# Kernel optimization log

Hardware: AMD Instinct MI355X
Metric: run time of the kernel (lower is better)

Reference implementation:

```python
import jax, jax.numpy as jnp
import numpy as np

DS_STEPS = 9
MAX_RND = 1.0
SMOKE_AUG = 0.5
SIZE = 512


def diamond_square(key, steps=DS_STEPS, max_rnd=MAX_RND):
    """Vectorized, faithful port of f_seed_grid + f_dsmain.

    Notes on faithfulness to the original code:
      - interior 'temp' reads in the diamond step resolve to the cell's own
        center (i_min + half == i_mid), exactly as in the original (buggy)
        indexing, so the interior averages double-count the center.
      - the '== 0' guards mean top/left edge midpoints are only written for
        the first row/column of cells (fresh zeros); elsewhere they were
        already written as bottom/right edges of neighboring cells.
    All per-level updates read only square-step (center) and coarser-level
    values, so each level is fully parallel.
    """
    N = 2 ** steps + 1
    hm = jnp.zeros((N, N), jnp.float32)
    corners = jax.random.uniform(jax.random.fold_in(key, 1000), (4,), minval=-1.0, maxval=1.0)
    hm = (hm.at[0, 0].set(corners[0]).at[0, -1].set(corners[1])
            .at[-1, 0].set(corners[2]).at[-1, -1].set(corners[3]))
    L = N - 1  # shape_length
    for level in range(steps):
        g = 2 ** level          # grid_split
        h = L // 2              # half_v_grid_size
        r = max_rnd / (level + 1)
        ks = jax.random.split(jax.random.fold_in(key, level), 5)
        lows = jnp.arange(g) * L
        highs = lows + L
        mids = lows + h
        # corner reads (set at coarser levels / seeds)
        nw = hm[lows[:, None], lows[None, :]]
        ne = hm[lows[:, None], highs[None, :]]
        sw = hm[highs[:, None], lows[None, :]]
        se = hm[highs[:, None], highs[None, :]]
        # square step: cell centers
        centers = (nw + ne + sw + se) / 4.0 + jax.random.uniform(ks[0], (g, g), minval=-r, maxval=r)
        hm = hm.at[mids[:, None], mids[None, :]].set(centers)
        # diamond step (all reads from post-square values)
        # top row (only i_min==0 cells pass the ==0 guard); temp = hm[max_index-h, j_mid] = centers[g-1, j]
        top = (centers[0, :] + hm[0, lows] + hm[0, highs] + centers[g - 1, :]) / 4.0 \
              + jax.random.uniform(ks[1], (g,), minval=-r, maxval=r)
        # left col (only j_min==0 cells); temp = hm[i_mid, max_index-h] = centers[i, g-1]
        left = (centers[:, 0] + hm[lows, 0] + hm[highs, 0] + centers[:, g - 1]) / 4.0 \
               + jax.random.uniform(ks[2], (g,), minval=-r, maxval=r)
        # right edges of every cell; interior temp == own center, boundary temp = centers[i, 0]
        temp_r = jnp.where(jnp.arange(g)[None, :] < g - 1, centers, centers[:, :1])
        right = (centers + ne + se + temp_r) / 4.0 + jax.random.uniform(ks[3], (g, g), minval=-r, maxval=r)
        # bottom edges of every cell; interior temp == own center, boundary temp = centers[0, j]
        temp_b = jnp.where(jnp.arange(g)[:, None] < g - 1, centers, centers[:1, :])
        bottom = (centers + sw + se + temp_b) / 4.0 + jax.random.uniform(ks[4], (g, g), minval=-r, maxval=r)
        hm = hm.at[0, mids].set(top)
        hm = hm.at[mids, 0].set(left)
        hm = hm.at[mids[:, None], highs[None, :]].set(right)
        hm = hm.at[highs[:, None], mids[None, :]].set(bottom)
        L //= 2
    return hm


def make_smoke_noise(key):
    hm = diamond_square(key)
    noise = (hm - hm.min()) / (hm.max() - hm.min())          # [513, 513] in [0,1]
    noise = jax.image.resize(noise, (SIZE, SIZE), method="bilinear")
    return noise * SMOKE_AUG                                  # [H, W]


def setup_inputs() -> dict:
    key = jax.random.key(0)
    img = jax.random.uniform(key, (32, 3, 512, 512), dtype=jnp.float32)
    return {"img": img}


def reference(img) -> jnp.ndarray:
    rn = make_smoke_noise(jax.random.key(42))                 # [H, W]
    rn = rn[None, None]                                       # broadcast over [B, C, H, W]
    return jnp.clip(img * (1.0 - rn) + rn, 0.0, 1.0)
```

## Files before the change

kernel.cpp:

```cpp
#include <hip/hip_runtime.h>

struct KP { unsigned a, b; };

__host__ __device__ constexpr unsigned rotl32(unsigned x, int d) {
  return (x << d) | (x >> (32 - d));
}

__host__ __device__ constexpr KP tf2x32(unsigned k0, unsigned k1, unsigned x0, unsigned x1) {
  unsigned k2 = k0 ^ k1 ^ 0x1BD11BDAu;
  unsigned v0 = x0 + k0;
  unsigned v1 = x1 + k1;
  const int R[5][4] = {{13,15,26,6},{17,29,16,24},{13,15,26,6},{17,29,16,24},{13,15,26,6}};
  const unsigned KI[5][2] = {{k1, k2 + 1u},{k2, k0 + 2u},{k0, k1 + 3u},{k1, k2 + 4u},{k2, k0 + 5u}};
  for (int g = 0; g < 5; ++g) {
    for (int r = 0; r < 4; ++r) {
      v0 += v1;
      v1 = rotl32(v1, R[g][r]);
      v1 ^= v0;
    }
    v0 += KI[g][0];
    v1 += KI[g][1];
  }
  return KP{v0, v1};
}

struct AllKeys {
  unsigned lk[9][5][2];
  unsigned ck[2];
};

__host__ __device__ constexpr AllKeys make_keys() {
  AllKeys K{};
  for (int l = 0; l < 9; ++l) {
    KP base = tf2x32(0u, 42u, 0u, (unsigned)l);
    for (int m = 0; m < 5; ++m) {
      KP s = tf2x32(base.a, base.b, 0u, (unsigned)m);
      K.lk[l][m][0] = s.a;
      K.lk[l][m][1] = s.b;
    }
  }
  KP ck = tf2x32(0u, 42u, 0u, 1000u);
  K.ck[0] = ck.a;
  K.ck[1] = ck.b;
  return K;
}

constexpr AllKeys KEYS = make_keys();

#define NG 513

__device__ inline unsigned rbits(unsigned k0, unsigned k1, unsigned i) {
  KP o = tf2x32(k0, k1, 0u, i);
  return o.a ^ o.b;
}

__device__ inline float bits_to_u(unsigned b, float r) {
  float u = __uint_as_float((b >> 9) | 0x3f800000u) - 1.0f;
  return fmaxf(-r, u * (2.0f * r) - r);
}

__device__ inline float draw_u(const unsigned* kk, unsigned i, float r) {
  return bits_to_u(rbits(kk[0], kk[1], i), r);
}

__device__ inline float cell_center(const float* hm, int level, int g, int L,
                                    int a, int b, float r) {
  int lo_i = a * L, hi_i = lo_i + L, lo_j = b * L, hi_j = lo_j + L;
  float nw = hm[lo_i * NG + lo_j], ne = hm[lo_i * NG + hi_j];
  float sw = hm[hi_i * NG + lo_j], se = hm[hi_i * NG + hi_j];
  return (nw + ne + sw + se) * 0.25f +
         draw_u(KEYS.lk[level][0], (unsigned)(a * g + b), r);
}

__device__ inline void do_cell(float* hm, int level, int i, int j) {
  int g = 1 << level;
  int L = 512 >> level;
  int h = L >> 1;
  float r = 1.0f / (float)(level + 1);
  int lo_i = i * L, hi_i = lo_i + L, mi_i = lo_i + h;
  int lo_j = j * L, hi_j = lo_j + L, mi_j = lo_j + h;
  float nw = hm[lo_i * NG + lo_j], ne = hm[lo_i * NG + hi_j];
  float sw = hm[hi_i * NG + lo_j], se = hm[hi_i * NG + hi_j];
  unsigned m = (unsigned)(i * g + j);

  float c = (nw + ne + sw + se) * 0.25f + draw_u(KEYS.lk[level][0], m, r);
  hm[mi_i * NG + mi_j] = c;

  float tr = (j < g - 1) ? c : cell_center(hm, level, g, L, i, 0, r);
  float right = (c + ne + se + tr) * 0.25f + draw_u(KEYS.lk[level][3], m, r);
  hm[mi_i * NG + hi_j] = right;

  float tb = (i < g - 1) ? c : cell_center(hm, level, g, L, 0, j, r);
  float bottom = (c + sw + se + tb) * 0.25f + draw_u(KEYS.lk[level][4], m, r);
  hm[hi_i * NG + mi_j] = bottom;

  if (i == 0) {
    float cg1 = (g == 1) ? c : cell_center(hm, level, g, L, g - 1, j, r);
    float top = (c + hm[lo_j] + hm[hi_j] + cg1) * 0.25f +
                draw_u(KEYS.lk[level][1], (unsigned)j, r);
    hm[mi_j] = top;
  }
  if (j == 0) {
    float cg1 = (g == 1) ? c : cell_center(hm, level, g, L, i, g - 1, r);
    float left = (c + hm[lo_i * NG] + hm[hi_i * NG] + cg1) * 0.25f +
                 draw_u(KEYS.lk[level][2], (unsigned)i, r);
    hm[mi_i * NG] = left;
  }
}

__global__ void k_ds_small(float* hm, unsigned* mmx) {
  int tid = threadIdx.x;
  if (tid == 0) {
#pragma unroll
    for (int q = 0; q < 4; ++q) {
      float v = bits_to_u(rbits(KEYS.ck[0], KEYS.ck[1], (unsigned)q), 1.0f);
      int y = (q >> 1) ? 512 : 0;
      int x = (q & 1) ? 512 : 0;
      hm[y * NG + x] = v;
    }
    mmx[0] = 0xFFFFFFFFu;
    mmx[1] = 0u;
  }
  __syncthreads();
  for (int lvl = 0; lvl <= 5; ++lvl) {
    int g = 1 << lvl;
    if (tid < g * g) do_cell(hm, lvl, tid >> lvl, tid & (g - 1));
    __syncthreads();
  }
}

__global__ void k_level(float* hm, int level) {
  int g = 1 << level;
  int gt = blockIdx.x * blockDim.x + threadIdx.x;
  do_cell(hm, level, gt >> level, gt & (g - 1));
}

__device__ inline unsigned enc_f(float f) {
  unsigned u = __float_as_uint(f);
  return (u & 0x80000000u) ? ~u : (u | 0x80000000u);
}
__device__ inline float dec_f(unsigned e) {
  unsigned u = (e & 0x80000000u) ? (e & 0x7FFFFFFFu) : ~e;
  return __uint_as_float(u);
}

__global__ void k_minmax(const float* hm, unsigned* mmx) {
  int gtid = blockIdx.x * blockDim.x + threadIdx.x;
  int nthreads = gridDim.x * blockDim.x;
  float mn = 3.4e38f, mx = -3.4e38f;
  for (int idx = gtid; idx < NG * NG; idx += nthreads) {
    float v = hm[idx];
    mn = fminf(mn, v);
    mx = fmaxf(mx, v);
  }
#pragma unroll
  for (int off = 32; off >= 1; off >>= 1) {
    mn = fminf(mn, __shfl_down(mn, off, 64));
    mx = fmaxf(mx, __shfl_down(mx, off, 64));
  }
  if ((threadIdx.x & 63) == 0) {
    atomicMin(&mmx[0], enc_f(mn));
    atomicMax(&mmx[1], enc_f(mx));
  }
}

__global__ void k_noise(const float* hm, const unsigned* mmx, float* rn) {
  int o = blockIdx.x * blockDim.x + threadIdx.x;
  int oy = o >> 9, ox = o & 511;
  const float csc = 512.0f / 513.0f;
  float dx = (float)(2 * ox + 1) * (1.0f / 1024.0f);
  float wx0 = 1.0f - dx * csc;
  float wx1 = 1.0f - (1.0f - dx) * csc;
  float sx = wx0 + wx1;
  wx0 /= sx; wx1 /= sx;
  float dy = (float)(2 * oy + 1) * (1.0f / 1024.0f);
  float wy0 = 1.0f - dy * csc;
  float wy1 = 1.0f - (1.0f - dy) * csc;
  float sy = wy0 + wy1;
  wy0 /= sy; wy1 /= sy;
  const float* r0 = hm + oy * NG + ox;
  float v = wy0 * (wx0 * r0[0] + wx1 * r0[1]) + wy1 * (wx0 * r0[NG] + wx1 * r0[NG + 1]);
  float mn = dec_f(mmx[0]), mx = dec_f(mmx[1]);
  rn[o] = 0.5f * ((v - mn) / (mx - mn));
}

__global__ void k_apply(const float4* __restrict__ img, const float* __restrict__ rn,
                        float4* __restrict__ out) {
  int t = blockIdx.x * blockDim.x + threadIdx.x;
  int pos4 = t & ((512 * 512 / 4) - 1);
  float4 a = img[t];
  float4 n = reinterpret_cast<const float4*>(rn)[pos4];
  float4 o;
  o.x = fminf(fmaxf(a.x * (1.0f - n.x) + n.x, 0.0f), 1.0f);
  o.y = fminf(fmaxf(a.y * (1.0f - n.y) + n.y, 0.0f), 1.0f);
  o.z = fminf(fmaxf(a.z * (1.0f - n.z) + n.z, 0.0f), 1.0f);
  o.w = fminf(fmaxf(a.w * (1.0f - n.w) + n.w, 0.0f), 1.0f);
  out[t] = o;
}

__global__ void k_apply_direct(const float* __restrict__ img, const float* __restrict__ hm,
                               const unsigned* __restrict__ mmx, float* __restrict__ out) {
  int t = blockIdx.x * blockDim.x + threadIdx.x;
  int pos = t & (512 * 512 - 1);
  int oy = pos >> 9, ox = pos & 511;
  const float csc = 512.0f / 513.0f;
  float dx = (float)(2 * ox + 1) * (1.0f / 1024.0f);
  float wx0 = 1.0f - dx * csc;
  float wx1 = 1.0f - (1.0f - dx) * csc;
  float sx = wx0 + wx1;
  wx0 /= sx; wx1 /= sx;
  float dy = (float)(2 * oy + 1) * (1.0f / 1024.0f);
  float wy0 = 1.0f - dy * csc;
  float wy1 = 1.0f - (1.0f - dy) * csc;
  float sy = wy0 + wy1;
  wy0 /= sy; wy1 /= sy;
  const float* r0 = hm + oy * NG + ox;
  float v = wy0 * (wx0 * r0[0] + wx1 * r0[1]) + wy1 * (wx0 * r0[NG] + wx1 * r0[NG + 1]);
  float mn = dec_f(mmx[0]), mx = dec_f(mmx[1]);
  float rnv = 0.5f * ((v - mn) / (mx - mn));
  float a = img[t];
  out[t] = fminf(fmaxf(a * (1.0f - rnv) + rnv, 0.0f), 1.0f);
}

extern "C" void kernel_launch(void* const* d_in, const int* in_sizes, int n_in,
                              void* d_out, int out_size, void* d_ws, size_t ws_size,
                              hipStream_t stream) {
  const float* img = (const float*)d_in[0];
  float* out = (float*)d_out;
  unsigned char* ws = (unsigned char*)d_ws;

  const size_t RN_BYTES = 512 * 512 * sizeof(float);
  const size_t HM_BYTES = NG * NG * sizeof(float);
  const size_t need_full = 16 + RN_BYTES + HM_BYTES;

  unsigned* mmx = (unsigned*)ws;
  bool use_rn = (ws_size >= need_full);
  float* rn = (float*)(ws + 16);
  float* hm = use_rn ? (float*)(ws + 16 + RN_BYTES) : (float*)(ws + 16);

  hipLaunchKernelGGL(k_ds_small, dim3(1), dim3(1024), 0, stream, hm, mmx);
  hipLaunchKernelGGL(k_level, dim3(16), dim3(256), 0, stream, hm, 6);
  hipLaunchKernelGGL(k_level, dim3(64), dim3(256), 0, stream, hm, 7);
  hipLaunchKernelGGL(k_level, dim3(256), dim3(256), 0, stream, hm, 8);
  hipLaunchKernelGGL(k_minmax, dim3(64), dim3(256), 0, stream, hm, mmx);

  const int total = 32 * 3 * 512 * 512;
  if (use_rn) {
    hipLaunchKernelGGL(k_noise, dim3(512 * 512 / 256), dim3(256), 0, stream, hm, mmx, rn);
    hipLaunchKernelGGL(k_apply, dim3(total / 4 / 256), dim3(256), 0, stream,
                       (const float4*)img, rn, (float4*)out);
  } else {
    hipLaunchKernelGGL(k_apply_direct, dim3(total / 256), dim3(256), 0, stream,
                       img, hm, mmx, out);
  }
}
```

Before: 218.0 us.

## Fuse min/max into diamond-square levels and noise resize into apply kernel

Each diamond-square cell now tracks the running min and max of the values it writes. A wave shuffle, shared-memory and atomic reduction at the end of each level kernel replaces the separate full-grid min/max pass. Level 6 is folded into the single-block small-level kernel, and the bilinear resize plus normalization is computed inline in a float4 apply kernel, which removes the intermediate noise buffer and two launches. The cost is that the bilinear weights and unaligned heightmap loads are recomputed for every batch and channel in the bandwidth-bound apply pass, and level 6 now runs on a single workgroup.

Measured after the change: 227.5 us. 4.4% more time.

```diff
diff --git a/kernel.cpp b/kernel.cpp
--- a/kernel.cpp
+++ b/kernel.cpp
@@ -63,6 +63,15 @@
   return bits_to_u(rbits(kk[0], kk[1], i), r);
 }
 
+__device__ inline unsigned enc_f(float f) {
+  unsigned u = __float_as_uint(f);
+  return (u & 0x80000000u) ? ~u : (u | 0x80000000u);
+}
+__device__ inline float dec_f(unsigned e) {
+  unsigned u = (e & 0x80000000u) ? (e & 0x7FFFFFFFu) : ~e;
+  return __uint_as_float(u);
+}
+
 __device__ inline float cell_center(const float* hm, int level, int g, int L,
                                     int a, int b, float r) {
   int lo_i = a * L, hi_i = lo_i + L, lo_j = b * L, hi_j = lo_j + L;
@@ -72,7 +81,8 @@
          draw_u(KEYS.lk[level][0], (unsigned)(a * g + b), r);
 }
 
-__device__ inline void do_cell(float* hm, int level, int i, int j) {
+__device__ inline void do_cell(float* hm, int level, int i, int j,
+                               float& mn, float& mx) {
   int g = 1 << level;
   int L = 512 >> level;
   int h = L >> 1;
@@ -85,141 +95,127 @@
 
   float c = (nw + ne + sw + se) * 0.25f + draw_u(KEYS.lk[level][0], m, r);
   hm[mi_i * NG + mi_j] = c;
+  mn = fminf(mn, c); mx = fmaxf(mx, c);
 
   float tr = (j < g - 1) ? c : cell_center(hm, level, g, L, i, 0, r);
   float right = (c + ne + se + tr) * 0.25f + draw_u(KEYS.lk[level][3], m, r);
   hm[mi_i * NG + hi_j] = right;
+  mn = fminf(mn, right); mx = fmaxf(mx, right);
 
   float tb = (i < g - 1) ? c : cell_center(hm, level, g, L, 0, j, r);
   float bottom = (c + sw + se + tb) * 0.25f + draw_u(KEYS.lk[level][4], m, r);
   hm[hi_i * NG + mi_j] = bottom;
+  mn = fminf(mn, bottom); mx = fmaxf(mx, bottom);
 
   if (i == 0) {
     float cg1 = (g == 1) ? c : cell_center(hm, level, g, L, g - 1, j, r);
     float top = (c + hm[lo_j] + hm[hi_j] + cg1) * 0.25f +
                 draw_u(KEYS.lk[level][1], (unsigned)j, r);
     hm[mi_j] = top;
+    mn = fminf(mn, top); mx = fmaxf(mx, top);
   }
   if (j == 0) {
     float cg1 = (g == 1) ? c : cell_center(hm, level, g, L, i, g - 1, r);
     float left = (c + hm[lo_i * NG] + hm[hi_i * NG] + cg1) * 0.25f +
                  draw_u(KEYS.lk[level][2], (unsigned)i, r);
     hm[mi_i * NG] = left;
-  }
-}
-
-__global__ void k_ds_small(float* hm, unsigned* mmx) {
-  int tid = threadIdx.x;
-  if (tid == 0) {
-#pragma unroll
-    for (int q = 0; q < 4; ++q) {
-      float v = bits_to_u(rbits(KEYS.ck[0], KEYS.ck[1], (unsigned)q), 1.0f);
-      int y = (q >> 1) ? 512 : 0;
-      int x = (q & 1) ? 512 : 0;
-      hm[y * NG + x] = v;
-    }
-    mmx[0] = 0xFFFFFFFFu;
-    mmx[1] = 0u;
-  }
-  __syncthreads();
-  for (int lvl = 0; lvl <= 5; ++lvl) {
-    int g = 1 << lvl;
-    if (tid < g * g) do_cell(hm, lvl, tid >> lvl, tid & (g - 1));
-    __syncthreads();
-  }
-}
-
-__global__ void k_level(float* hm, int level) {
-  int g = 1 << level;
-  int gt = blockIdx.x * blockDim.x + threadIdx.x;
-  do_cell(hm, level, gt >> level, gt & (g - 1));
-}
-
-__device__ inline unsigned enc_f(float f) {
-  unsigned u = __float_as_uint(f);
-  return (u & 0x80000000u) ? ~u : (u | 0x80000000u);
-}
-__device__ inline float dec_f(unsigned e) {
-  unsigned u = (e & 0x80000000u) ? (e & 0x7FFFFFFFu) : ~e;
-  return __uint_as_float(u);
-}
-
-__global__ void k_minmax(const float* hm, unsigned* mmx) {
-  int gtid = blockIdx.x * blockDim.x + threadIdx.x;
-  int nthreads = gridDim.x * blockDim.x;
-  float mn = 3.4e38f, mx = -3.4e38f;
-  for (int idx = gtid; idx < NG * NG; idx += nthreads) {
-    float v = hm[idx];
-    mn = fminf(mn, v);
-    mx = fmaxf(mx, v);
-  }
+    mn = fminf(mn, left); mx = fmaxf(mx, left);
+  }
+}
+
+template <int NWAVES>
+__device__ inline void block_minmax_atomic(float mn, float mx, unsigned* mmx) {
+  __shared__ float smn[NWAVES], smx[NWAVES];
 #pragma unroll
   for (int off = 32; off >= 1; off >>= 1) {
     mn = fminf(mn, __shfl_down(mn, off, 64));
     mx = fmaxf(mx, __shfl_down(mx, off, 64));
   }
-  if ((threadIdx.x & 63) == 0) {
+  int lane = threadIdx.x & 63, w = threadIdx.x >> 6;
+  if (lane == 0) { smn[w] = mn; smx[w] = mx; }
+  __syncthreads();
+  if (threadIdx.x == 0) {
+#pragma unroll
+    for (int q = 1; q < NWAVES; ++q) {
+      mn = fminf(mn, smn[q]);
+      mx = fmaxf(mx, smx[q]);
+    }
     atomicMin(&mmx[0], enc_f(mn));
     atomicMax(&mmx[1], enc_f(mx));
   }
 }
 
-__global__ void k_noise(const float* hm, const unsigned* mmx, float* rn) {
-  int o = blockIdx.x * blockDim.x + threadIdx.x;
-  int oy = o >> 9, ox = o & 511;
+__global__ void k_ds_small(float* hm, unsigned* mmx) {
+  int tid = threadIdx.x;
+  float mn = 3.4e38f, mx = -3.4e38f;
+  if (tid == 0) {
+    mmx[0] = 0xFFFFFFFFu;
+    mmx[1] = 0u;
+  }
+  if (tid < 4) {
+    float v = bits_to_u(rbits(KEYS.ck[0], KEYS.ck[1], (unsigned)tid), 1.0f);
+    int y = (tid >> 1) ? 512 : 0;
+    int x = (tid & 1) ? 512 : 0;
+    hm[y * NG + x] = v;
+    mn = fminf(mn, v); mx = fmaxf(mx, v);
+  }
+  __syncthreads();
+  for (int lvl = 0; lvl <= 5; ++lvl) {
+    int g = 1 << lvl;
+    if (tid < g * g) do_cell(hm, lvl, tid >> lvl, tid & (g - 1), mn, mx);
+    __syncthreads();
+  }
+  for (int c = tid; c < 64 * 64; c += 1024)
+    do_cell(hm, 6, c >> 6, c & 63, mn, mx);
+  block_minmax_atomic<16>(mn, mx, mmx);
+}
+
+__global__ void k_level(float* hm, unsigned* mmx, int level) {
+  int g = 1 << level;
+  int gt = blockIdx.x * blockDim.x + threadIdx.x;
+  float mn = 3.4e38f, mx = -3.4e38f;
+  do_cell(hm, level, gt >> level, gt & (g - 1), mn, mx);
+  block_minmax_atomic<4>(mn, mx, mmx);
+}
+
+__global__ void k_apply(const float4* __restrict__ img, const float* __restrict__ hm,
+                        const unsigned* __restrict__ mmx, float4* __restrict__ out) {
+  int t = blockIdx.x * blockDim.x + threadIdx.x;
+  int pos4 = t & (512 * 512 / 4 - 1);
+  int oy = pos4 >> 7;
+  int ox = (pos4 & 127) << 2;
+
+  float mn = dec_f(mmx[0]);
+  float scale = 0.5f / (dec_f(mmx[1]) - mn);
+
   const float csc = 512.0f / 513.0f;
-  float dx = (float)(2 * ox + 1) * (1.0f / 1024.0f);
-  float wx0 = 1.0f - dx * csc;
-  float wx1 = 1.0f - (1.0f - dx) * csc;
-  float sx = wx0 + wx1;
-  wx0 /= sx; wx1 /= sx;
   float dy = (float)(2 * oy + 1) * (1.0f / 1024.0f);
   float wy0 = 1.0f - dy * csc;
   float wy1 = 1.0f - (1.0f - dy) * csc;
   float sy = wy0 + wy1;
   wy0 /= sy; wy1 /= sy;
+
   const float* r0 = hm + oy * NG + ox;
-  float v = wy0 * (wx0 * r0[0] + wx1 * r0[1]) + wy1 * (wx0 * r0[NG] + wx1 * r0[NG + 1]);
-  float mn = dec_f(mmx[0]), mx = dec_f(mmx[1]);
-  rn[o] = 0.5f * ((v - mn) / (mx - mn));
-}
-
-__global__ void k_apply(const float4* __restrict__ img, const float* __restrict__ rn,
-                        float4* __restrict__ out) {
-  int t = blockIdx.x * blockDim.x + threadIdx.x;
-  int pos4 = t & ((512 * 512 / 4) - 1);
+  float n[4];
+#pragma unroll
+  for (int k = 0; k < 4; ++k) {
+    float dx = (float)(2 * (ox + k) + 1) * (1.0f / 1024.0f);
+    float wx0 = 1.0f - dx * csc;
+    float wx1 = 1.0f - (1.0f - dx) * csc;
+    float sx = wx0 + wx1;
+    wx0 /= sx; wx1 /= sx;
+    float v = wy0 * (wx0 * r0[k] + wx1 * r0[k + 1]) +
+              wy1 * (wx0 * r0[NG + k] + wx1 * r0[NG + k + 1]);
+    n[k] = (v - mn) * scale;
+  }
+
   float4 a = img[t];
-  float4 n = reinterpret_cast<const float4*>(rn)[pos4];
   float4 o;
-  o.x = fminf(fmaxf(a.x * (1.0f - n.x) + n.x, 0.0f), 1.0f);
-  o.y = fminf(fmaxf(a.y * (1.0f - n.y) + n.y, 0.0f), 1.0f);
-  o.z = fminf(fmaxf(a.z * (1.0f - n.z) + n.z, 0.0f), 1.0f);
-  o.w = fminf(fmaxf(a.w * (1.0f - n.w) + n.w, 0.0f), 1.0f);
+  o.x = fminf(fmaxf(a.x * (1.0f - n[0]) + n[0], 0.0f), 1.0f);
+  o.y = fminf(fmaxf(a.y * (1.0f - n[1]) + n[1], 0.0f), 1.0f);
+  o.z = fminf(fmaxf(a.z * (1.0f - n[2]) + n[2], 0.0f), 1.0f);
+  o.w = fminf(fmaxf(a.w * (1.0f - n[3]) + n[3], 0.0f), 1.0f);
   out[t] = o;
-}
-
-__global__ void k_apply_direct(const float* __restrict__ img, const float* __restrict__ hm,
-                               const unsigned* __restrict__ mmx, float* __restrict__ out) {
-  int t = blockIdx.x * blockDim.x + threadIdx.x;
-  int pos = t & (512 * 512 - 1);
-  int oy = pos >> 9, ox = pos & 511;
-  const float csc = 512.0f / 513.0f;
-  float dx = (float)(2 * ox + 1) * (1.0f / 1024.0f);
-  float wx0 = 1.0f - dx * csc;
-  float wx1 = 1.0f - (1.0f - dx) * csc;
-  float sx = wx0 + wx1;
-  wx0 /= sx; wx1 /= sx;
-  float dy = (float)(2 * oy + 1) * (1.0f / 1024.0f);
-  float wy0 = 1.0f - dy * csc;
-  float wy1 = 1.0f - (1.0f - dy) * csc;
-  float sy = wy0 + wy1;
-  wy0 /= sy; wy1 /= sy;
-  const float* r0 = hm + oy * NG + ox;
-  float v = wy0 * (wx0 * r0[0] + wx1 * r0[1]) + wy1 * (wx0 * r0[NG] + wx1 * r0[NG + 1]);
-  float mn = dec_f(mmx[0]), mx = dec_f(mmx[1]);
-  float rnv = 0.5f * ((v - mn) / (mx - mn));
-  float a = img[t];
-  out[t] = fminf(fmaxf(a * (1.0f - rnv) + rnv, 0.0f), 1.0f);
 }
 
 extern "C" void kernel_launch(void* const* d_in, const int* in_sizes, int n_in,
@@ -229,28 +225,14 @@
   float* out = (float*)d_out;
   unsigned char* ws = (unsigned char*)d_ws;
 
-  const size_t RN_BYTES = 512 * 512 * sizeof(float);
-  const size_t HM_BYTES = NG * NG * sizeof(float);
-  const size_t need_full = 16 + RN_BYTES + HM_BYTES;
-
   unsigned* mmx = (unsigned*)ws;
-  bool use_rn = (ws_size >= need_full);
-  float* rn = (float*)(ws + 16);
-  float* hm = use_rn ? (float*)(ws + 16 + RN_BYTES) : (float*)(ws + 16);
+  float* hm = (float*)(ws + 16);
 
   hipLaunchKernelGGL(k_ds_small, dim3(1), dim3(1024), 0, stream, hm, mmx);
-  hipLaunchKernelGGL(k_level, dim3(16), dim3(256), 0, stream, hm, 6);
-  hipLaunchKernelGGL(k_level, dim3(64), dim3(256), 0, stream, hm, 7);
-  hipLaunchKernelGGL(k_level, dim3(256), dim3(256), 0, stream, hm, 8);
-  hipLaunchKernelGGL(k_minmax, dim3(64), dim3(256), 0, stream, hm, mmx);
+  hipLaunchKernelGGL(k_level, dim3(64), dim3(256), 0, stream, hm, mmx, 7);
+  hipLaunchKernelGGL(k_level, dim3(256), dim3(256), 0, stream, hm, mmx, 8);
 
   const int total = 32 * 3 * 512 * 512;
-  if (use_rn) {
-    hipLaunchKernelGGL(k_noise, dim3(512 * 512 / 256), dim3(256), 0, stream, hm, mmx, rn);
-    hipLaunchKernelGGL(k_apply, dim3(total / 4 / 256), dim3(256), 0, stream,
-                       (const float4*)img, rn, (float4*)out);
-  } else {
-    hipLaunchKernelGGL(k_apply_direct, dim3(total / 256), dim3(256), 0, stream,
-                       img, hm, mmx, out);
-  }
-}
+  hipLaunchKernelGGL(k_apply, dim3(total / 4 / 256), dim3(256), 0, stream,
+                     (const float4*)img, hm, mmx, (float4*)out);
+}
```
